# Kernel tuning notes

Measured on AMD Instinct MI355X. Metric: run time of the kernel, lower is better.

## Reference

```python
import jax, jax.numpy as jnp
import numpy as np

HID = 1024
HEADS = 16
HEAD_DIM = HID // HEADS

def setup_inputs() -> dict:
    key = jax.random.key(0)
    ks = jax.random.split(key, 12)
    B, S = 4, 2048
    inp = {
        'query': jax.random.normal(ks[0], (B, S, HID), dtype=jnp.float32),
        'key':   jax.random.normal(ks[1], (B, S, HID), dtype=jnp.float32),
        'value': jax.random.normal(ks[2], (B, S, HID), dtype=jnp.float32),
        'mask':  jax.random.randint(ks[3], (B, S, S), 0, 2, dtype=jnp.int32),
        'Wq': jax.random.normal(ks[4], (HID, HID), dtype=jnp.float32) * (1.0 / np.sqrt(HID)),
        'bq': jnp.zeros((HID,), dtype=jnp.float32),
        'Wk': jax.random.normal(ks[5], (HID, HID), dtype=jnp.float32) * (1.0 / np.sqrt(HID)),
        'bk': jnp.zeros((HID,), dtype=jnp.float32),
        'Wv': jax.random.normal(ks[6], (HID, HID), dtype=jnp.float32) * (1.0 / np.sqrt(HID)),
        'bv': jnp.zeros((HID,), dtype=jnp.float32),
        'Wo': jax.random.normal(ks[7], (HID, HID), dtype=jnp.float32) * (1.0 / np.sqrt(HID)),
        'bo': jnp.zeros((HID,), dtype=jnp.float32),
    }
    return inp

def _split_heads(x, W, b):
    # x: [B,S,HID] -> [B,H,S,Dh]
    B, S, _ = x.shape
    y = x @ W + b
    return y.reshape(B, S, HEADS, HEAD_DIM).transpose(0, 2, 1, 3)

def reference(query, key, value, mask, Wq, bq, Wk, bk, Wv, bv, Wo, bo):
    B, S, _ = query.shape
    Q = _split_heads(query, Wq, bq)
    K = _split_heads(key, Wk, bk)
    V = _split_heads(value, Wv, bv)
    scale = 1.0 / jnp.sqrt(jnp.asarray(HEAD_DIM, dtype=Q.dtype))
    energy = jnp.einsum('bhqd,bhkd->bhqk', Q, K) * scale  # [B,H,S,S]
    m = mask[:, None, :, :]  # unsqueeze(1)
    energy = jnp.where(m == 0, jnp.asarray(-1e9, dtype=energy.dtype), energy)
    attn = jax.nn.softmax(energy, axis=-1)
    out = jnp.einsum('bhqk,bhkd->bhqd', attn, V)  # [B,H,S,Dh]
    out = out.transpose(0, 2, 1, 3).reshape(B, S, HID)  # merge heads
    return out @ Wo + bo
```

## Files before the change

### kernel.cpp

```cpp
#include <hip/hip_runtime.h>
#include <hip/hip_bf16.h>
#include <stdint.h>

typedef unsigned short u16;
typedef __attribute__((ext_vector_type(4))) float f32x4;
typedef __attribute__((ext_vector_type(8))) short bf16x8;

#define HID 1024
#define NHEADS 16
#define HD 64
#define BATCH 4
#define SEQ 2048
#define NROWS (BATCH * SEQ)

#define QSCALE 0.18033688011112042f

__device__ __forceinline__ u16 f2b(float f) {
  uint32_t u = __float_as_uint(f);
  u += 0x7fffu + ((u >> 16) & 1u);
  return (u16)(u >> 16);
}

__device__ __forceinline__ u16 bfbits(float f) {
  __hip_bfloat16 h = __float2bfloat16(f);
  return *reinterpret_cast<u16*>(&h);
}

__device__ __forceinline__ void gload_lds16(const void* g, void* l) {
  __builtin_amdgcn_global_load_lds((__attribute__((address_space(1))) void*)g,
                                   (__attribute__((address_space(3))) void*)l, 16, 0, 0);
}

__global__ __launch_bounds__(256) void k_pack_mask(const int* __restrict__ mask,
                                                   uint32_t* __restrict__ bits) {
  size_t wid = ((size_t)blockIdx.x * 256 + threadIdx.x) >> 6;
  int lane = threadIdx.x & 63;
  int v = mask[wid * 64 + lane];
  unsigned long long bal = __ballot(v != 0);
  if (lane == 0) ((unsigned long long*)bits)[wid] = bal;
}

struct Cvt3 { const float* src[3]; u16* dst[3]; };
__global__ __launch_bounds__(256) void k_cvt3(Cvt3 c, int n4) {
  int i = blockIdx.x * 256 + threadIdx.x;
  if (i >= n4) return;
  int z = blockIdx.y;
  float4 v = ((const float4*)c.src[z])[i];
  ushort4 o;
  o.x = f2b(v.x); o.y = f2b(v.y); o.z = f2b(v.z); o.w = f2b(v.w);
  ((ushort4*)c.dst[z])[i] = o;
}

struct Wt4 { const float* W[4]; u16* Wt[4]; };
__global__ __launch_bounds__(256) void k_wtrans4(Wt4 a) {
  __shared__ float t[64][65];
  int z = blockIdx.z;
  const float* W = a.W[z];
  u16* Wt = a.Wt[z];
  int bx = blockIdx.x * 64;
  int by = blockIdx.y * 64;
  int tid = threadIdx.x;
  int r = tid >> 2, c0 = (tid & 3) * 16;
#pragma unroll
  for (int j = 0; j < 16; j += 4) {
    float4 v = *(const float4*)&W[(size_t)(bx + r) * HID + by + c0 + j];
    t[r][c0 + j] = v.x; t[r][c0 + j + 1] = v.y;
    t[r][c0 + j + 2] = v.z; t[r][c0 + j + 3] = v.w;
  }
  __syncthreads();
#pragma unroll
  for (int j = 0; j < 16; ++j)
    Wt[(size_t)(by + r) * HID + bx + c0 + j] = f2b(t[c0 + j][r]);
}

__device__ __forceinline__ void gemm_core(const u16* __restrict__ A, const u16* __restrict__ Bt,
                                          u16* As, u16* Bs, int m0, int n0,
                                          f32x4 (&acc)[4][4]) {
  const int tid = threadIdx.x, wave = tid >> 6, lane = tid & 63;
  const int g = lane >> 4, c16 = lane & 15;
  const int wm = (wave & 1) * 64, wn = (wave >> 1) * 64;
  const int lr = lane >> 3, lc = lane & 7;
  const int swz = lc ^ lr;

  for (int it = 0; it < 16; ++it) {
    const int k0 = it * 64;
#pragma unroll
    for (int t = 0; t < 8; ++t) {
      int idx = wave * 8 + t;
      if (idx < 16) {
        const u16* src = A + (size_t)(m0 + idx * 8 + lr) * HID + k0 + swz * 8;
        gload_lds16(src, &As[idx * 512]);
      } else {
        int c = idx - 16;
        const u16* src = Bt + (size_t)(n0 + c * 8 + lr) * HID + k0 + swz * 8;
        gload_lds16(src, &Bs[c * 512]);
      }
    }
    __syncthreads();
    bf16x8 af[2][4], bfr[2][4];
#pragma unroll
    for (int s = 0; s < 2; ++s) {
#pragma unroll
      for (int f = 0; f < 4; ++f) {
        int rowa = wm + f * 16 + c16;
        af[s][f] = *(const bf16x8*)&As[rowa * 64 + (((s * 4 + g) ^ (rowa & 7)) * 8)];
        int rowb = wn + f * 16 + c16;
        bfr[s][f] = *(const bf16x8*)&Bs[rowb * 64 + (((s * 4 + g) ^ (rowb & 7)) * 8)];
      }
    }
#pragma unroll
    for (int s = 0; s < 2; ++s)
#pragma unroll
      for (int mf = 0; mf < 4; ++mf)
#pragma unroll
        for (int nf = 0; nf < 4; ++nf)
          acc[mf][nf] = __builtin_amdgcn_mfma_f32_16x16x32_bf16(af[s][mf], bfr[s][nf],
                                                                acc[mf][nf], 0, 0, 0);
    __syncthreads();
  }
}

struct GemmSet {
  const u16* A[3]; const u16* Bt[3]; const float* bias[3];
  u16* out[3]; float scale[3]; int mode[3];
};
__global__ __launch_bounds__(256) void k_gemm_qkv(GemmSet gs) {
  __shared__ __align__(16) u16 As[128 * 64];
  __shared__ __align__(16) u16 Bs[128 * 64];
  const int z = blockIdx.z;
  const int tid = threadIdx.x, wave = tid >> 6, lane = tid & 63;
  const int g = lane >> 4, c16 = lane & 15;
  const int m0 = blockIdx.x * 128, n0 = blockIdx.y * 128;
  const int wm = (wave & 1) * 64, wn = (wave >> 1) * 64;
  f32x4 acc[4][4] = {};
  gemm_core(gs.A[z], gs.Bt[z], As, Bs, m0, n0, acc);

  const float scale = gs.scale[z];
  u16* ob = gs.out[z];
  float bv[4];
#pragma unroll
  for (int nf = 0; nf < 4; ++nf) bv[nf] = gs.bias[z][n0 + wn + nf * 16 + c16];

  if (gs.mode[z] == 0) {
#pragma unroll
    for (int mf = 0; mf < 4; ++mf)
#pragma unroll
      for (int nf = 0; nf < 4; ++nf)
#pragma unroll
        for (int r = 0; r < 4; ++r) {
          int m = m0 + wm + mf * 16 + 4 * g + r;
          int n = n0 + wn + nf * 16 + c16;
          ob[(size_t)m * HID + n] = f2b((acc[mf][nf][r] + bv[nf]) * scale);
        }
  } else {
#pragma unroll
    for (int mf = 0; mf < 4; ++mf)
#pragma unroll
      for (int nf = 0; nf < 4; ++nf)
#pragma unroll
        for (int r = 0; r < 4; ++r) {
          int m = m0 + wm + mf * 16 + 4 * g + r;
          int n = n0 + wn + nf * 16 + c16;
          int b = m >> 11, s_ = m & 2047, hh = n >> 6, d = n & 63;
          ob[(size_t)((b * NHEADS + hh) * HD + d) * SEQ + s_] = f2b(acc[mf][nf][r] + bv[nf]);
        }
  }
}

__global__ __launch_bounds__(256) void k_gemmo(const u16* __restrict__ A, const u16* __restrict__ Bt,
                                               const float* __restrict__ bias, float* __restrict__ out) {
  __shared__ __align__(16) u16 As[128 * 64];
  __shared__ __align__(16) u16 Bs[128 * 64];
  const int tid = threadIdx.x, wave = tid >> 6, lane = tid & 63;
  const int g = lane >> 4, c16 = lane & 15;
  const int m0 = blockIdx.x * 128, n0 = blockIdx.y * 128;
  const int wm = (wave & 1) * 64, wn = (wave >> 1) * 64;
  f32x4 acc[4][4] = {};
  gemm_core(A, Bt, As, Bs, m0, n0, acc);

  float bv[4];
#pragma unroll
  for (int nf = 0; nf < 4; ++nf) bv[nf] = bias[n0 + wn + nf * 16 + c16];
#pragma unroll
  for (int mf = 0; mf < 4; ++mf)
#pragma unroll
    for (int nf = 0; nf < 4; ++nf)
#pragma unroll
      for (int r = 0; r < 4; ++r) {
        int m = m0 + wm + mf * 16 + 4 * g + r;
        int n = n0 + wn + nf * 16 + c16;
        out[(size_t)m * HID + n] = acc[mf][nf][r] + bv[nf];
      }
}

__global__ __launch_bounds__(256) void k_attn(const u16* __restrict__ Qb, const u16* __restrict__ Kb,
                                              const u16* __restrict__ Vtb, const uint32_t* __restrict__ mb,
                                              u16* __restrict__ Ob) {
  __shared__ __align__(16) u16 Ks[64 * 64];
  __shared__ __align__(16) u16 Vs[64 * 64];
  __shared__ __align__(16) u16 Ps[4][16 * 72];
  const int tid = threadIdx.x, wave = tid >> 6, lane = tid & 63;
  const int g = lane >> 4, c16 = lane & 15;
  const int bh = blockIdx.y, b = bh >> 4, h = bh & 15;
  const int qw = blockIdx.x * 64 + wave * 16;
  const int lr = lane >> 3, lc = lane & 7;
  const int swz = lc ^ lr;

  bf16x8 qa[2];
  {
    const u16* qp = Qb + (size_t)(b * SEQ + qw + c16) * HID + h * HD + 8 * g;
    qa[0] = *(const bf16x8*)qp;
    qa[1] = *(const bf16x8*)(qp + 32);
  }
  float lrun[4] = {0.f, 0.f, 0.f, 0.f};
  f32x4 o[4];
#pragma unroll
  for (int df = 0; df < 4; ++df) o[df] = f32x4{0.f, 0.f, 0.f, 0.f};

  const uint32_t* mwp = mb + (size_t)(b * SEQ + qw + 4 * g) * 64;
  u16* Pw = &Ps[wave][0];
  const int pbase = 4 * g * 72 + c16;

  for (int it = 0; it < 32; ++it) {
    const int kv0 = it * 64;
#pragma unroll
    for (int t = 0; t < 4; ++t) {
      int idx = wave * 4 + t;
      if (idx < 8) {
        const u16* src = Kb + (size_t)(b * SEQ + kv0 + idx * 8 + lr) * HID + h * HD + swz * 8;
        gload_lds16(src, &Ks[idx * 512]);
      } else {
        int c = idx - 8;
        const u16* src = Vtb + (size_t)(bh * HD + c * 8 + lr) * SEQ + kv0 + swz * 8;
        gload_lds16(src, &Vs[c * 512]);
      }
    }
    __syncthreads();

    f32x4 sc[4] = {};
#pragma unroll
    for (int s = 0; s < 2; ++s)
#pragma unroll
      for (int nf = 0; nf < 4; ++nf) {
        int row = nf * 16 + c16;
        bf16x8 kb = *(const bf16x8*)&Ks[row * 64 + (((s * 4 + g) ^ (row & 7)) * 8)];
        sc[nf] = __builtin_amdgcn_mfma_f32_16x16x32_bf16(qa[s], kb, sc[nf], 0, 0, 0);
      }

#pragma unroll
    for (int r = 0; r < 4; ++r) {
      uint2 w = *(const uint2*)(mwp + (size_t)r * 64 + it * 2);
      uint32_t a0 = w.x >> c16;
      uint32_t a1 = w.y >> c16;
      float p0 = exp2f(sc[0][r]) * (float)(a0 & 1u);
      float p1 = exp2f(sc[1][r]) * (float)((a0 >> 16) & 1u);
      float p2 = exp2f(sc[2][r]) * (float)(a1 & 1u);
      float p3 = exp2f(sc[3][r]) * (float)((a1 >> 16) & 1u);
      lrun[r] += (p0 + p1) + (p2 + p3);
      int rowoff = pbase + r * 72;
      Pw[rowoff]      = bfbits(p0);
      Pw[rowoff + 16] = bfbits(p1);
      Pw[rowoff + 32] = bfbits(p2);
      Pw[rowoff + 48] = bfbits(p3);
    }
    __asm__ volatile("s_waitcnt lgkmcnt(0)" ::: "memory");
    bf16x8 pa[2];
    pa[0] = *(const bf16x8*)&Pw[c16 * 72 + 8 * g];
    pa[1] = *(const bf16x8*)&Pw[c16 * 72 + 32 + 8 * g];

#pragma unroll
    for (int s = 0; s < 2; ++s)
#pragma unroll
      for (int df = 0; df < 4; ++df) {
        int row = df * 16 + c16;
        bf16x8 vb = *(const bf16x8*)&Vs[row * 64 + (((s * 4 + g) ^ (row & 7)) * 8)];
        o[df] = __builtin_amdgcn_mfma_f32_16x16x32_bf16(pa[s], vb, o[df], 0, 0, 0);
      }
    __syncthreads();
  }

#pragma unroll
  for (int r = 0; r < 4; ++r) {
#pragma unroll
    for (int off = 1; off < 16; off <<= 1) lrun[r] += __shfl_xor(lrun[r], off);
  }

#pragma unroll
  for (int df = 0; df < 4; ++df)
#pragma unroll
    for (int r = 0; r < 4; ++r) {
      int q = qw + 4 * g + r;
      int d = df * 16 + c16;
      Ob[(size_t)(b * SEQ + q) * HID + h * HD + d] = f2b(o[df][r] / lrun[r]);
    }
}

extern "C" void kernel_launch(void* const* d_in, const int* in_sizes, int n_in,
                              void* d_out, int out_size, void* d_ws, size_t ws_size,
                              hipStream_t stream) {
  const float* query = (const float*)d_in[0];
  const float* key   = (const float*)d_in[1];
  const float* value = (const float*)d_in[2];
  const int*   mask  = (const int*)d_in[3];
  const float* Wq = (const float*)d_in[4];
  const float* bq = (const float*)d_in[5];
  const float* Wk = (const float*)d_in[6];
  const float* bk = (const float*)d_in[7];
  const float* Wv = (const float*)d_in[8];
  const float* bv = (const float*)d_in[9];
  const float* Wo = (const float*)d_in[10];
  const float* bo = (const float*)d_in[11];

  char* ws = (char*)d_ws;
  const size_t MB = 1024 * 1024;
  u16* Wtq = (u16*)(ws + 0 * MB);
  u16* Wtk = (u16*)(ws + 2 * MB);
  u16* Wtv = (u16*)(ws + 4 * MB);
  u16* Wto = (u16*)(ws + 6 * MB);
  uint32_t* mbits = (uint32_t*)(ws + 8 * MB);
  u16* Qb  = (u16*)(ws + 10 * MB);
  u16* Kb  = (u16*)(ws + 26 * MB);
  u16* Vtb = (u16*)(ws + 42 * MB);
  u16* Xq  = (u16*)(ws + 58 * MB);
  u16* Xk  = (u16*)(ws + 74 * MB);
  u16* Xv  = (u16*)(ws + 90 * MB);
  u16* Ob  = Xq;
  const bool merged = ws_size >= 106 * MB;

  k_pack_mask<<<dim3(65536), dim3(256), 0, stream>>>(mask, mbits);
  Wt4 wa = {{Wq, Wk, Wv, Wo}, {Wtq, Wtk, Wtv, Wto}};
  k_wtrans4<<<dim3(16, 16, 4), 256, 0, stream>>>(wa);

  const int n4 = NROWS * HID / 4;
  if (merged) {
    Cvt3 cv = {{query, key, value}, {Xq, Xk, Xv}};
    k_cvt3<<<dim3(n4 / 256, 3), 256, 0, stream>>>(cv, n4);
    GemmSet gs = {{Xq, Xk, Xv}, {Wtq, Wtk, Wtv}, {bq, bk, bv},
                  {Qb, Kb, Vtb}, {QSCALE, 1.0f, 1.0f}, {0, 0, 1}};
    k_gemm_qkv<<<dim3(64, 8, 3), 256, 0, stream>>>(gs);
  } else {
    const float* srcs[3] = {query, key, value};
    const float* bs[3] = {bq, bk, bv};
    u16* outs[3] = {Qb, Kb, Vtb};
    float scs[3] = {QSCALE, 1.0f, 1.0f};
    int mds[3] = {0, 0, 1};
    for (int i = 0; i < 3; ++i) {
      Cvt3 cv = {{srcs[i], nullptr, nullptr}, {Xq, nullptr, nullptr}};
      k_cvt3<<<dim3(n4 / 256, 1), 256, 0, stream>>>(cv, n4);
      GemmSet gs = {{Xq, nullptr, nullptr}, {Wtq == nullptr ? nullptr : (i == 0 ? Wtq : (i == 1 ? Wtk : Wtv)), nullptr, nullptr},
                    {bs[i], nullptr, nullptr}, {outs[i], nullptr, nullptr},
                    {scs[i], 0.f, 0.f}, {mds[i], 0, 0}};
      k_gemm_qkv<<<dim3(64, 8, 1), 256, 0, stream>>>(gs);
    }
  }

  k_attn<<<dim3(32, 64), 256, 0, stream>>>(Qb, Kb, Vtb, mbits, Ob);

  k_gemmo<<<dim3(64, 8), 256, 0, stream>>>(Ob, Wto, bo, (float*)d_out);
}
```

Measured before the change: 473.8 us.

## Double-buffer K/V tiles in attention and compute row sums via MFMA

The attention kernel now double-buffers the K and V shared-memory tiles, prefetching the next tile while the current one is computed, and drops one barrier per iteration. Row sums of P are accumulated with an extra MFMA against a ones vector instead of scalar adds and a shuffle reduction. Other changes: mask words are loaded early, MFMA sections run under raised wave priority, exp2 and reciprocal use hardware intrinsics, and launch bounds request 4 blocks per CU. Doubling LDS for K/V may limit occupancy, and the fast intrinsics slightly change rounding. The per-head weight selection in the fallback host path is also simplified.

```diff
diff --git a/kernel.cpp b/kernel.cpp
--- a/kernel.cpp
+++ b/kernel.cpp
@@ -193,11 +193,11 @@
       }
 }
 
-__global__ __launch_bounds__(256) void k_attn(const u16* __restrict__ Qb, const u16* __restrict__ Kb,
-                                              const u16* __restrict__ Vtb, const uint32_t* __restrict__ mb,
-                                              u16* __restrict__ Ob) {
-  __shared__ __align__(16) u16 Ks[64 * 64];
-  __shared__ __align__(16) u16 Vs[64 * 64];
+__global__ __launch_bounds__(256, 4) void k_attn(const u16* __restrict__ Qb, const u16* __restrict__ Kb,
+                                                 const u16* __restrict__ Vtb, const uint32_t* __restrict__ mb,
+                                                 u16* __restrict__ Ob) {
+  __shared__ __align__(16) u16 Ks[2][64 * 64];
+  __shared__ __align__(16) u16 Vs[2][64 * 64];
   __shared__ __align__(16) u16 Ps[4][16 * 72];
   const int tid = threadIdx.x, wave = tid >> 6, lane = tid & 63;
   const int g = lane >> 4, c16 = lane & 15;
@@ -206,57 +206,73 @@
   const int lr = lane >> 3, lc = lane & 7;
   const int swz = lc ^ lr;
 
+  const u16* kbase = Kb + (size_t)(b * SEQ + (wave * 4 % 8) * 8 + lr) * HID + h * HD + swz * 8;
+  const u16* vbase = Vtb + (size_t)(bh * HD + ((wave * 4) & 7) * 8 + lr) * SEQ + swz * 8;
+
   bf16x8 qa[2];
   {
     const u16* qp = Qb + (size_t)(b * SEQ + qw + c16) * HID + h * HD + 8 * g;
     qa[0] = *(const bf16x8*)qp;
     qa[1] = *(const bf16x8*)(qp + 32);
   }
-  float lrun[4] = {0.f, 0.f, 0.f, 0.f};
-  f32x4 o[4];
+  f32x4 o[4], lacc;
 #pragma unroll
   for (int df = 0; df < 4; ++df) o[df] = f32x4{0.f, 0.f, 0.f, 0.f};
+  lacc = f32x4{0.f, 0.f, 0.f, 0.f};
+  const bf16x8 ones = {0x3F80, 0x3F80, 0x3F80, 0x3F80, 0x3F80, 0x3F80, 0x3F80, 0x3F80};
 
   const uint32_t* mwp = mb + (size_t)(b * SEQ + qw + 4 * g) * 64;
   u16* Pw = &Ps[wave][0];
   const int pbase = 4 * g * 72 + c16;
 
-  for (int it = 0; it < 32; ++it) {
+  auto STAGE = [&](int it, int buf) {
     const int kv0 = it * 64;
 #pragma unroll
     for (int t = 0; t < 4; ++t) {
       int idx = wave * 4 + t;
       if (idx < 8) {
         const u16* src = Kb + (size_t)(b * SEQ + kv0 + idx * 8 + lr) * HID + h * HD + swz * 8;
-        gload_lds16(src, &Ks[idx * 512]);
+        gload_lds16(src, &Ks[buf][idx * 512]);
       } else {
         int c = idx - 8;
         const u16* src = Vtb + (size_t)(bh * HD + c * 8 + lr) * SEQ + kv0 + swz * 8;
-        gload_lds16(src, &Vs[c * 512]);
-      }
-    }
-    __syncthreads();
+        gload_lds16(src, &Vs[buf][c * 512]);
+      }
+    }
+  };
+
+  STAGE(0, 0);
+  __syncthreads();
+
+#pragma unroll 2
+  for (int it = 0; it < 32; ++it) {
+    const int buf = it & 1;
+    if (it + 1 < 32) STAGE(it + 1, buf ^ 1);
+
+    uint2 w[4];
+#pragma unroll
+    for (int r = 0; r < 4; ++r) w[r] = *(const uint2*)(mwp + (size_t)r * 64 + it * 2);
 
     f32x4 sc[4] = {};
+    __builtin_amdgcn_s_setprio(1);
 #pragma unroll
     for (int s = 0; s < 2; ++s)
 #pragma unroll
       for (int nf = 0; nf < 4; ++nf) {
         int row = nf * 16 + c16;
-        bf16x8 kb = *(const bf16x8*)&Ks[row * 64 + (((s * 4 + g) ^ (row & 7)) * 8)];
+        bf16x8 kb = *(const bf16x8*)&Ks[buf][row * 64 + (((s * 4 + g) ^ (row & 7)) * 8)];
         sc[nf] = __builtin_amdgcn_mfma_f32_16x16x32_bf16(qa[s], kb, sc[nf], 0, 0, 0);
       }
+    __builtin_amdgcn_s_setprio(0);
 
 #pragma unroll
     for (int r = 0; r < 4; ++r) {
-      uint2 w = *(const uint2*)(mwp + (size_t)r * 64 + it * 2);
-      uint32_t a0 = w.x >> c16;
-      uint32_t a1 = w.y >> c16;
-      float p0 = exp2f(sc[0][r]) * (float)(a0 & 1u);
-      float p1 = exp2f(sc[1][r]) * (float)((a0 >> 16) & 1u);
-      float p2 = exp2f(sc[2][r]) * (float)(a1 & 1u);
-      float p3 = exp2f(sc[3][r]) * (float)((a1 >> 16) & 1u);
-      lrun[r] += (p0 + p1) + (p2 + p3);
+      uint32_t a0 = w[r].x >> c16;
+      uint32_t a1 = w[r].y >> c16;
+      float p0 = __builtin_amdgcn_exp2f(sc[0][r]) * (float)(a0 & 1u);
+      float p1 = __builtin_amdgcn_exp2f(sc[1][r]) * (float)((a0 >> 16) & 1u);
+      float p2 = __builtin_amdgcn_exp2f(sc[2][r]) * (float)(a1 & 1u);
+      float p3 = __builtin_amdgcn_exp2f(sc[3][r]) * (float)((a1 >> 16) & 1u);
       int rowoff = pbase + r * 72;
       Pw[rowoff]      = bfbits(p0);
       Pw[rowoff + 16] = bfbits(p1);
@@ -268,31 +284,31 @@
     pa[0] = *(const bf16x8*)&Pw[c16 * 72 + 8 * g];
     pa[1] = *(const bf16x8*)&Pw[c16 * 72 + 32 + 8 * g];
 
-#pragma unroll
-    for (int s = 0; s < 2; ++s)
+    __builtin_amdgcn_s_setprio(1);
+#pragma unroll
+    for (int s = 0; s < 2; ++s) {
 #pragma unroll
       for (int df = 0; df < 4; ++df) {
         int row = df * 16 + c16;
-        bf16x8 vb = *(const bf16x8*)&Vs[row * 64 + (((s * 4 + g) ^ (row & 7)) * 8)];
+        bf16x8 vb = *(const bf16x8*)&Vs[buf][row * 64 + (((s * 4 + g) ^ (row & 7)) * 8)];
         o[df] = __builtin_amdgcn_mfma_f32_16x16x32_bf16(pa[s], vb, o[df], 0, 0, 0);
       }
+      lacc = __builtin_amdgcn_mfma_f32_16x16x32_bf16(pa[s], ones, lacc, 0, 0, 0);
+    }
+    __builtin_amdgcn_s_setprio(0);
     __syncthreads();
   }
 
 #pragma unroll
   for (int r = 0; r < 4; ++r) {
-#pragma unroll
-    for (int off = 1; off < 16; off <<= 1) lrun[r] += __shfl_xor(lrun[r], off);
-  }
-
-#pragma unroll
-  for (int df = 0; df < 4; ++df)
-#pragma unroll
-    for (int r = 0; r < 4; ++r) {
+    float rl = __builtin_amdgcn_rcpf(lacc[r]);
+#pragma unroll
+    for (int df = 0; df < 4; ++df) {
       int q = qw + 4 * g + r;
       int d = df * 16 + c16;
-      Ob[(size_t)(b * SEQ + q) * HID + h * HD + d] = f2b(o[df][r] / lrun[r]);
-    }
+      Ob[(size_t)(b * SEQ + q) * HID + h * HD + d] = bfbits(o[df][r] * rl);
+    }
+  }
 }
 
 extern "C" void kernel_launch(void* const* d_in, const int* in_sizes, int n_in,
@@ -340,6 +356,7 @@
     k_gemm_qkv<<<dim3(64, 8, 3), 256, 0, stream>>>(gs);
   } else {
     const float* srcs[3] = {query, key, value};
+    const u16* wts[3] = {Wtq, Wtk, Wtv};
     const float* bs[3] = {bq, bk, bv};
     u16* outs[3] = {Qb, Kb, Vtb};
     float scs[3] = {QSCALE, 1.0f, 1.0f};
@@ -347,7 +364,7 @@
     for (int i = 0; i < 3; ++i) {
       Cvt3 cv = {{srcs[i], nullptr, nullptr}, {Xq, nullptr, nullptr}};
       k_cvt3<<<dim3(n4 / 256, 1), 256, 0, stream>>>(cv, n4);
-      GemmSet gs = {{Xq, nullptr, nullptr}, {Wtq == nullptr ? nullptr : (i == 0 ? Wtq : (i == 1 ? Wtk : Wtv)), nullptr, nullptr},
+      GemmSet gs = {{Xq, nullptr, nullptr}, {wts[i], nullptr, nullptr},
                     {bs[i], nullptr, nullptr}, {outs[i], nullptr, nullptr},
                     {scs[i], 0.f, 0.f}, {mds[i], 0, 0}};
       k_gemm_qkv<<<dim3(64, 8, 1), 256, 0, stream>>>(gs);
```

Result: faster. 448.3 us (-5.4%).
